# Kernel tuning notes

Hardware: AMD Instinct MI355X
Metric: run time of the kernel (lower is better)

Reference implementation:

```python
import jax, jax.numpy as jnp
import numpy as np

B, G = 128, 20000
HID = 64
NUM_BINS = 10
LEAKY_SLOPE = 0.01  # torch nn.LeakyReLU default


def setup_inputs() -> dict:
    key = jax.random.key(0)
    k1, k2, k3, k4, k5, k6 = jax.random.split(key, 6)
    vals = jax.random.normal(k1, (B, G), dtype=jnp.float32)
    keep = jax.random.uniform(k2, (B, G)) < 0.1
    expr_value = jnp.where(keep, vals, 0.0)
    # MLP params: Linear(1 -> HID), Linear(HID -> NUM_BINS-1)
    W1 = jax.random.normal(k3, (1, HID), dtype=jnp.float32) * 0.5
    b1 = jax.random.normal(k4, (HID,), dtype=jnp.float32) * 0.1
    W2 = jax.random.normal(k5, (HID, NUM_BINS - 1), dtype=jnp.float32) * (1.0 / np.sqrt(HID))
    b2 = jax.random.normal(k6, (NUM_BINS - 1,), dtype=jnp.float32) * 0.1
    return {"expr_value": expr_value, "W1": W1, "b1": b1, "W2": W2, "b2": b2}


def reference(expr_value, W1, b1, W2, b2):
    # mask of nonzero expression positions (B, G)
    mask_expr = (expr_value != 0).astype(jnp.float32)
    # tiny MLP applied to every position (vectorized; zero positions masked out below)
    x = expr_value[..., None]                      # (B, G, 1)
    h = x * W1[0] + b1                             # (B, G, HID); Linear(1->HID)
    h = jnp.where(h >= 0, h, LEAKY_SLOPE * h)      # LeakyReLU
    logits = jnp.einsum('bgh,hk->bgk', h, W2) + b2 # (B, G, NUM_BINS-1)
    p = jax.nn.softmax(logits, axis=-1)            # softmax over bins 1..num_bins-1
    m = mask_expr[..., None]
    # bin 0 prob = 1 where expr==0 else 0; bins 1.. = softmax where expr!=0 else 0
    probs = jnp.concatenate([1.0 - m, p * m], axis=-1)  # (B, G, NUM_BINS)
    return probs, mask_expr
```

## Files before the change

kernel.cpp:

```cpp
#include <hip/hip_runtime.h>
#include <math.h>

#define HID 64
#define KB 9
#define NB 10
#define NTOT (128 * 20000)
#define EPT 4
#define BLOCK 256
#define LEAKY 0.01f
#define RSTRIDE 20
#define TAB_FLOATS (128 + 65 * RSTRIDE)
#define WS_BYTES (TAB_FLOATS * 4)
#define SENT 3.0e38f

__device__ __forceinline__ void build_table(
    const float* __restrict__ W1, const float* __restrict__ b1,
    const float* __restrict__ W2, const float* __restrict__ b2,
    int tid, float* ts , float* tab ,
    float* st, float* sw, float* sb, float* tsrt)
{
    if (tid < HID) {
        float w = W1[tid], b = b1[tid];
        st[tid] = (w != 0.0f) ? (-b / w) : -SENT;
        sw[tid] = w; sb[tid] = b;
    }
    __syncthreads();
    if (tid < HID) {
        float t = st[tid];
        int r = 0;
        for (int i = 0; i < HID; ++i) {
            float ti = st[i];
            r += (ti < t || (ti == t && i < tid)) ? 1 : 0;
        }
        tsrt[r] = t;
    }
    __syncthreads();
    if (tid < 128) ts[tid] = (tid < HID) ? tsrt[tid] : SENT;
    for (int item = tid; item < 65 * KB; item += BLOCK) {
        int r = item / KB, k = item - r * KB;
        float xm;
        if (r == 0)        xm = tsrt[0] - 1.0f;
        else if (r == HID) xm = tsrt[HID - 1] + 1.0f;
        else               xm = 0.5f * (tsrt[r - 1] + tsrt[r]);
        float A = 0.0f, C = b2[k];
        for (int j = 0; j < HID; ++j) {
            float w = sw[j], bb = sb[j];
            float s = (fmaf(w, xm, bb) >= 0.0f) ? 1.0f : LEAKY;
            float w2s = W2[j * KB + k] * s;
            A = fmaf(w2s, w, A);
            C = fmaf(w2s, bb, C);
        }
        tab[r * RSTRIDE + k] = A;
        tab[r * RSTRIDE + KB + k] = C;
    }
    __syncthreads();
}

__device__ __forceinline__ void compute_elems(
    const float* __restrict__ expr, float* __restrict__ out,
    const float* ts, const float* tab, int i0)
{
    const float4 xv = *(const float4*)(expr + i0);
    float x[EPT] = {xv.x, xv.y, xv.z, xv.w};
    float o[EPT * NB];
    float msk[EPT];
    #pragma unroll
    for (int e = 0; e < EPT; ++e) {
        const float xe = x[e];
        int idx = 0;
        #pragma unroll
        for (int s = 64; s >= 1; s >>= 1)
            idx += (ts[idx + s - 1] <= xe) ? s : 0;
        const float* row = tab + idx * RSTRIDE;
        float lg[KB];
        #pragma unroll
        for (int k = 0; k < KB; ++k) lg[k] = fmaf(row[k], xe, row[KB + k]);
        float m = lg[0];
        #pragma unroll
        for (int k = 1; k < KB; ++k) m = fmaxf(m, lg[k]);
        float p[KB];
        float s = 0.0f;
        #pragma unroll
        for (int k = 0; k < KB; ++k) { p[k] = __expf(lg[k] - m); s += p[k]; }
        const float r = __frcp_rn(s);
        const bool nz = (xe != 0.0f);
        msk[e] = nz ? 1.0f : 0.0f;
        o[e * NB] = nz ? 0.0f : 1.0f;
        #pragma unroll
        for (int k = 0; k < KB; ++k) o[e * NB + 1 + k] = nz ? p[k] * r : 0.0f;
    }
    float4* dst = (float4*)(out + (size_t)i0 * NB);
    #pragma unroll
    for (int q = 0; q < EPT * NB / 4; ++q) dst[q] = ((const float4*)o)[q];
    float4* mdst = (float4*)(out + (size_t)NTOT * NB + i0);
    *mdst = make_float4(msk[0], msk[1], msk[2], msk[3]);
}

__global__ __launch_bounds__(BLOCK) void setup_kernel(
    const float* __restrict__ W1, const float* __restrict__ b1,
    const float* __restrict__ W2, const float* __restrict__ b2,
    float* __restrict__ ws)
{
    __shared__ float st[HID], sw[HID], sb[HID], tsrt[HID];
    build_table(W1, b1, W2, b2, threadIdx.x, ws, ws + 128, st, sw, sb, tsrt);
}

__global__ __launch_bounds__(BLOCK) void main_kernel(
    const float* __restrict__ expr, const float* __restrict__ ws,
    float* __restrict__ out)
{
    __shared__ float ts[128];
    __shared__ float tab[65 * RSTRIDE];
    const int tid = threadIdx.x;
    for (int t = tid; t < TAB_FLOATS; t += BLOCK) {
        float v = ws[t];
        if (t < 128) ts[t] = v; else tab[t - 128] = v;
    }
    __syncthreads();
    const int i0 = (blockIdx.x * BLOCK + tid) * EPT;
    compute_elems(expr, out, ts, tab, i0);
}

__global__ __launch_bounds__(BLOCK) void fused_kernel(
    const float* __restrict__ expr,
    const float* __restrict__ W1, const float* __restrict__ b1,
    const float* __restrict__ W2, const float* __restrict__ b2,
    float* __restrict__ out)
{
    __shared__ float ts[128];
    __shared__ float tab[65 * RSTRIDE];
    __shared__ float st[HID], sw[HID], sb[HID], tsrt[HID];
    build_table(W1, b1, W2, b2, threadIdx.x, ts, tab, st, sw, sb, tsrt);
    const int i0 = (blockIdx.x * BLOCK + threadIdx.x) * EPT;
    compute_elems(expr, out, ts, tab, i0);
}

extern "C" void kernel_launch(void* const* d_in, const int* in_sizes, int n_in,
                              void* d_out, int out_size, void* d_ws, size_t ws_size,
                              hipStream_t stream) {
    const float* expr = (const float*)d_in[0];
    const float* W1   = (const float*)d_in[1];
    const float* b1   = (const float*)d_in[2];
    const float* W2   = (const float*)d_in[3];
    const float* b2   = (const float*)d_in[4];
    float* out = (float*)d_out;
    const int nblocks = NTOT / (BLOCK * EPT);

    if (ws_size >= (size_t)WS_BYTES) {
        float* ws = (float*)d_ws;
        setup_kernel<<<1, BLOCK, 0, stream>>>(W1, b1, W2, b2, ws);
        main_kernel<<<nblocks, BLOCK, 0, stream>>>(expr, ws, out);
    } else {
        fused_kernel<<<nblocks, BLOCK, 0, stream>>>(expr, W1, b1, W2, b2, out);
    }
}
```

Baseline: 154.8 us.

## Parallelize table setup across blocks and stage output through LDS for coalesced stores

The setup kernel now runs 65 blocks of 64 threads, one block per table row. Each thread computes its hidden unit's contribution and a shared-memory reduction sums them, replacing the single-block serial loop over rows. The main kernel stages each thread's 40 output floats in a 40KB LDS buffer and writes them out block-contiguously, so each float4 store instruction is coalesced across the wavefront. The extra LDS use may reduce occupancy and adds a block-wide barrier before the stores.

Result: faster. 141.9 us (-8.4%).

```diff
diff --git a/kernel.cpp b/kernel.cpp
--- a/kernel.cpp
+++ b/kernel.cpp
@@ -13,12 +13,126 @@
 #define WS_BYTES (TAB_FLOATS * 4)
 #define SENT 3.0e38f
 
-__device__ __forceinline__ void build_table(
+__global__ __launch_bounds__(64) void setup_kernel(
     const float* __restrict__ W1, const float* __restrict__ b1,
     const float* __restrict__ W2, const float* __restrict__ b2,
-    int tid, float* ts , float* tab ,
-    float* st, float* sw, float* sb, float* tsrt)
+    float* __restrict__ ws)
 {
+    __shared__ float t_lds[HID], w_lds[HID], b_lds[HID], tsrt[HID];
+    __shared__ float w2_lds[HID * KB];
+    __shared__ float red[18 * 65];
+
+    const int j = threadIdx.x;
+    const int r = blockIdx.x;
+    const float w = W1[j], b = b1[j];
+    const float t = (w != 0.0f) ? (-b / w) : -SENT;
+    t_lds[j] = t; w_lds[j] = w; b_lds[j] = b;
+    #pragma unroll
+    for (int q = j; q < HID * KB; q += 64) w2_lds[q] = W2[q];
+    __syncthreads();
+
+    int rank = 0;
+    for (int i = 0; i < HID; ++i) {
+        float ti = t_lds[i];
+        rank += (ti < t || (ti == t && i < j)) ? 1 : 0;
+    }
+    tsrt[rank] = t;
+    __syncthreads();
+
+    float xm;
+    if (r == 0)        xm = tsrt[0] - 1.0f;
+    else if (r == HID) xm = tsrt[HID - 1] + 1.0f;
+    else               xm = 0.5f * (tsrt[r - 1] + tsrt[r]);
+
+    const float s = (fmaf(w, xm, b) >= 0.0f) ? 1.0f : LEAKY;
+    #pragma unroll
+    for (int k = 0; k < KB; ++k) {
+        const float w2s = w2_lds[j * KB + k] * s;
+        red[(2 * k) * 65 + j]     = w2s * w;
+        red[(2 * k + 1) * 65 + j] = w2s * b;
+    }
+    __syncthreads();
+
+    if (j < 18) {
+        float acc = 0.0f;
+        for (int i = 0; i < HID; ++i) acc += red[j * 65 + i];
+        const int k = j >> 1;
+        if (j & 1) ws[128 + r * RSTRIDE + KB + k] = acc + b2[k];
+        else       ws[128 + r * RSTRIDE + k]      = acc;
+    }
+    if (r == 0) { ws[j] = tsrt[j]; ws[64 + j] = SENT; }
+}
+
+__global__ __launch_bounds__(BLOCK) void main_kernel(
+    const float* __restrict__ expr, const float* __restrict__ ws,
+    float* __restrict__ out)
+{
+    __shared__ float ts[128];
+    __shared__ float tab[65 * RSTRIDE];
+    __shared__ float so[BLOCK * EPT * NB];
+
+    const int tid = threadIdx.x;
+    for (int t = tid; t < TAB_FLOATS; t += BLOCK) {
+        float v = ws[t];
+        if (t < 128) ts[t] = v; else tab[t - 128] = v;
+    }
+    __syncthreads();
+
+    const int i0 = (blockIdx.x * BLOCK + tid) * EPT;
+    const float4 xv = *(const float4*)(expr + i0);
+    float x[EPT] = {xv.x, xv.y, xv.z, xv.w};
+    float o[EPT * NB];
+    float msk[EPT];
+    #pragma unroll
+    for (int e = 0; e < EPT; ++e) {
+        const float xe = x[e];
+        int idx = 0;
+        #pragma unroll
+        for (int s = 64; s >= 1; s >>= 1)
+            idx += (ts[idx + s - 1] <= xe) ? s : 0;
+        const float* row = tab + idx * RSTRIDE;
+        float lg[KB];
+        #pragma unroll
+        for (int k = 0; k < KB; ++k) lg[k] = fmaf(row[k], xe, row[KB + k]);
+        float m = lg[0];
+        #pragma unroll
+        for (int k = 1; k < KB; ++k) m = fmaxf(m, lg[k]);
+        float p[KB];
+        float s = 0.0f;
+        #pragma unroll
+        for (int k = 0; k < KB; ++k) { p[k] = __expf(lg[k] - m); s += p[k]; }
+        const float rcp = __frcp_rn(s);
+        const bool nz = (xe != 0.0f);
+        msk[e] = nz ? 1.0f : 0.0f;
+        o[e * NB] = nz ? 0.0f : 1.0f;
+        #pragma unroll
+        for (int k = 0; k < KB; ++k) o[e * NB + 1 + k] = nz ? p[k] * rcp : 0.0f;
+    }
+
+    *(float4*)(out + (size_t)NTOT * NB + i0) = make_float4(msk[0], msk[1], msk[2], msk[3]);
+
+    #pragma unroll
+    for (int q = 0; q < NB; ++q)
+        ((float4*)so)[tid * NB + q] = ((const float4*)o)[q];
+    __syncthreads();
+    float* gout = out + (size_t)blockIdx.x * (BLOCK * EPT * NB);
+    #pragma unroll
+    for (int q = 0; q < NB; ++q) {
+        const int f4 = q * BLOCK + tid;
+        *(float4*)(gout + f4 * 4) = ((const float4*)so)[f4];
+    }
+}
+
+__global__ __launch_bounds__(BLOCK) void fused_kernel(
+    const float* __restrict__ expr,
+    const float* __restrict__ W1, const float* __restrict__ b1,
+    const float* __restrict__ W2, const float* __restrict__ b2,
+    float* __restrict__ out)
+{
+    __shared__ float ts[128];
+    __shared__ float tab[65 * RSTRIDE];
+    __shared__ float st[HID], sw[HID], sb[HID], tsrt[HID];
+    const int tid = threadIdx.x;
     if (tid < HID) {
         float w = W1[tid], b = b1[tid];
         st[tid] = (w != 0.0f) ? (-b / w) : -SENT;
@@ -54,23 +168,16 @@
         tab[r * RSTRIDE + KB + k] = C;
     }
     __syncthreads();
-}
-
-__device__ __forceinline__ void compute_elems(
-    const float* __restrict__ expr, float* __restrict__ out,
-    const float* ts, const float* tab, int i0)
-{
+    const int i0 = (blockIdx.x * BLOCK + tid) * EPT;
     const float4 xv = *(const float4*)(expr + i0);
     float x[EPT] = {xv.x, xv.y, xv.z, xv.w};
-    float o[EPT * NB];
-    float msk[EPT];
+    float o[EPT * NB]; float msk[EPT];
     #pragma unroll
     for (int e = 0; e < EPT; ++e) {
         const float xe = x[e];
         int idx = 0;
         #pragma unroll
-        for (int s = 64; s >= 1; s >>= 1)
-            idx += (ts[idx + s - 1] <= xe) ? s : 0;
+        for (int s = 64; s >= 1; s >>= 1) idx += (ts[idx + s - 1] <= xe) ? s : 0;
         const float* row = tab + idx * RSTRIDE;
         float lg[KB];
         #pragma unroll
@@ -78,61 +185,20 @@
         float m = lg[0];
         #pragma unroll
         for (int k = 1; k < KB; ++k) m = fmaxf(m, lg[k]);
-        float p[KB];
-        float s = 0.0f;
+        float p[KB]; float s = 0.0f;
         #pragma unroll
         for (int k = 0; k < KB; ++k) { p[k] = __expf(lg[k] - m); s += p[k]; }
-        const float r = __frcp_rn(s);
+        const float rcp = __frcp_rn(s);
         const bool nz = (xe != 0.0f);
         msk[e] = nz ? 1.0f : 0.0f;
         o[e * NB] = nz ? 0.0f : 1.0f;
         #pragma unroll
-        for (int k = 0; k < KB; ++k) o[e * NB + 1 + k] = nz ? p[k] * r : 0.0f;
+        for (int k = 0; k < KB; ++k) o[e * NB + 1 + k] = nz ? p[k] * rcp : 0.0f;
     }
     float4* dst = (float4*)(out + (size_t)i0 * NB);
     #pragma unroll
     for (int q = 0; q < EPT * NB / 4; ++q) dst[q] = ((const float4*)o)[q];
-    float4* mdst = (float4*)(out + (size_t)NTOT * NB + i0);
-    *mdst = make_float4(msk[0], msk[1], msk[2], msk[3]);
-}
-
-__global__ __launch_bounds__(BLOCK) void setup_kernel(
-    const float* __restrict__ W1, const float* __restrict__ b1,
-    const float* __restrict__ W2, const float* __restrict__ b2,
-    float* __restrict__ ws)
-{
-    __shared__ float st[HID], sw[HID], sb[HID], tsrt[HID];
-    build_table(W1, b1, W2, b2, threadIdx.x, ws, ws + 128, st, sw, sb, tsrt);
-}
-
-__global__ __launch_bounds__(BLOCK) void main_kernel(
-    const float* __restrict__ expr, const float* __restrict__ ws,
-    float* __restrict__ out)
-{
-    __shared__ float ts[128];
-    __shared__ float tab[65 * RSTRIDE];
-    const int tid = threadIdx.x;
-    for (int t = tid; t < TAB_FLOATS; t += BLOCK) {
-        float v = ws[t];
-        if (t < 128) ts[t] = v; else tab[t - 128] = v;
-    }
-    __syncthreads();
-    const int i0 = (blockIdx.x * BLOCK + tid) * EPT;
-    compute_elems(expr, out, ts, tab, i0);
-}
-
-__global__ __launch_bounds__(BLOCK) void fused_kernel(
-    const float* __restrict__ expr,
-    const float* __restrict__ W1, const float* __restrict__ b1,
-    const float* __restrict__ W2, const float* __restrict__ b2,
-    float* __restrict__ out)
-{
-    __shared__ float ts[128];
-    __shared__ float tab[65 * RSTRIDE];
-    __shared__ float st[HID], sw[HID], sb[HID], tsrt[HID];
-    build_table(W1, b1, W2, b2, threadIdx.x, ts, tab, st, sw, sb, tsrt);
-    const int i0 = (blockIdx.x * BLOCK + threadIdx.x) * EPT;
-    compute_elems(expr, out, ts, tab, i0);
+    *(float4*)(out + (size_t)NTOT * NB + i0) = make_float4(msk[0], msk[1], msk[2], msk[3]);
 }
 
 extern "C" void kernel_launch(void* const* d_in, const int* in_sizes, int n_in,
@@ -148,7 +214,7 @@
 
     if (ws_size >= (size_t)WS_BYTES) {
         float* ws = (float*)d_ws;
-        setup_kernel<<<1, BLOCK, 0, stream>>>(W1, b1, W2, b2, ws);
+        setup_kernel<<<65, 64, 0, stream>>>(W1, b1, W2, b2, ws);
         main_kernel<<<nblocks, BLOCK, 0, stream>>>(expr, ws, out);
     } else {
         fused_kernel<<<nblocks, BLOCK, 0, stream>>>(expr, W1, b1, W2, b2, out);
```
